# Kernel optimization log

Measured on AMD Instinct MI355X. Metric: run time of the kernel, lower is better.

## Reference

```python
import jax, jax.numpy as jnp
import numpy as np

B, S, F, D = 16384, 8, 16, 256
H, K, E, EH = 4, 16, 4, 128
ROWS = jnp.array([0, 0, 1, 1, 2, 2, 3, 3])
COLS = jnp.array([1, 3, 0, 2, 1, 3, 0, 2])
EPS = 1e-5


def setup_inputs() -> dict:
    key = jax.random.key(0)
    ks = jax.random.split(key, 16)
    s = lambda fan: 1.0 / np.sqrt(fan)
    return {
        "x": jax.random.normal(ks[0], (B, S, F), jnp.float32),
        "w_embed": jax.random.normal(ks[1], (F, D), jnp.float32) * s(F),
        "b_embed": jnp.zeros((D,), jnp.float32),
        "wq": jax.random.normal(ks[2], (D, H * K), jnp.float32) * s(D),
        "bq": jnp.zeros((H * K,), jnp.float32),
        "wk": jax.random.normal(ks[3], (D, H * K), jnp.float32) * s(D),
        "bk": jnp.zeros((H * K,), jnp.float32),
        "wv": jax.random.normal(ks[4], (D, H * K), jnp.float32) * s(D),
        "bv": jnp.zeros((H * K,), jnp.float32),
        "wo": jax.random.normal(ks[5], (H * K, D), jnp.float32) * s(H * K),
        "bo": jnp.zeros((D,), jnp.float32),
        "ln1_s": jnp.ones((D,), jnp.float32),
        "ln1_b": jnp.zeros((D,), jnp.float32),
        "wg": jax.random.normal(ks[6], (D, E), jnp.float32) * s(D),
        "bg": jnp.zeros((E,), jnp.float32),
        "w1": jax.random.normal(ks[7], (E, D, EH), jnp.float32) * s(D),
        "b1": jnp.zeros((E, EH), jnp.float32),
        "w2": jax.random.normal(ks[8], (E, EH, D), jnp.float32) * s(EH),
        "b2": jnp.zeros((E, D), jnp.float32),
        "ln2_s": jnp.ones((D,), jnp.float32),
        "ln2_b": jnp.zeros((D,), jnp.float32),
        "pad_vec": jax.random.normal(ks[9], (1, 1, 1, D), jnp.float32),
        "conv_w": jax.random.normal(ks[10], (3, 3, D, D), jnp.float32) * s(9 * D),
        "conv_b": jnp.zeros((D,), jnp.float32),
        "ln3_s": jnp.ones((D,), jnp.float32),
        "ln3_b": jnp.zeros((D,), jnp.float32),
    }


def _ln(x, scale, offset):
    m = jnp.mean(x, axis=-1, keepdims=True)
    v = jnp.mean(jnp.square(x - m), axis=-1, keepdims=True)
    return scale * (x - m) * jax.lax.rsqrt(v + EPS) + offset


def reference(x, w_embed, b_embed, wq, bq, wk, bk, wv, bv, wo, bo,
              ln1_s, ln1_b, wg, bg, w1, b1, w2, b2, ln2_s, ln2_b,
              pad_vec, conv_w, conv_b, ln3_s, ln3_b):
    # Stabilizer embedding: [B,S,F] -> [B,S,D]
    h = x @ w_embed + b_embed

    # Multi-head self-attention (haiku MultiHeadAttention semantics)
    q = (h @ wq + bq).reshape(B, S, H, K) / jnp.sqrt(jnp.asarray(K, h.dtype))
    k = (h @ wk + bk).reshape(B, S, H, K)
    v = (h @ wv + bv).reshape(B, S, H, K)
    logits = jnp.einsum('bqhk,bshk->bhqs', q, k)
    attn = jax.nn.softmax(logits, axis=-1)
    ctx = jnp.einsum('bhqs,bshk->bqhk', attn, v).reshape(B, S, H * K)
    attn_out = ctx @ wo + bo
    h = _ln(h + attn_out, ln1_s, ln1_b)

    # Dense mixture-of-experts with softmax combine
    gate = jax.nn.softmax(h @ wg + bg, axis=-1)                      # [B,S,E]
    hid = jax.nn.relu(jnp.einsum('bsd,edh->ebsh', h, w1) + b1[:, None, None, :])
    exp_out = jnp.einsum('ebsh,ehd->ebsd', hid, w2) + b2[:, None, None, :]
    moe = jnp.einsum('bse,ebsd->bsd', gate, exp_out)
    h = _ln(h + moe, ln2_s, ln2_b)

    # Scatter onto 4x4 grid, 3x3 SAME conv, gather back
    grid = jnp.tile(pad_vec, (B, 4, 4, 1))
    grid = grid.at[:, ROWS, COLS, :].set(h)
    grid_out = jax.lax.conv_general_dilated(
        grid, conv_w, window_strides=(1, 1), padding='SAME',
        dimension_numbers=('NHWC', 'HWIO', 'NHWC')) + conv_b
    conv_gathered = grid_out[:, ROWS, COLS, :]
    h = _ln(h + conv_gathered, ln3_s, ln3_b)
    return h
```

## Files before the change

kernel.cpp:

```cpp
#include <hip/hip_runtime.h>


typedef short bf16x8 __attribute__((ext_vector_type(8)));
typedef float f32x4 __attribute__((ext_vector_type(4)));

union FragU { uint4 u; bf16x8 h; };

#define MFMA(a, b, c) __builtin_amdgcn_mfma_f32_16x16x32_bf16((a), (b), (c), 0, 0, 0)

__device__ __forceinline__ unsigned short f2b(float f) {
  union { float f; unsigned int u; } x; x.f = f;
  unsigned int r = x.u + 0x7FFFu + ((x.u >> 16) & 1u);
  return (unsigned short)(r >> 16);
}

constexpr int FR_QKV  = 0;
constexpr int FR_WO   = 96;
constexpr int FR_W1   = 128;
constexpr int FR_W2   = 384;
constexpr int FR_CONV = 640;
constexpr int FR_TOT  = 1280;
constexpr size_t PADC_BYTE_OFF = (size_t)FR_TOT * 1024;

constexpr int OFF_HF = 0;
constexpr int OFF_ST = 33280;
constexpr int OFF_HB = 66560;
constexpr int OFF_MB = 83456;
constexpr int OFF_CB = 116736;
constexpr int OFF_G  = 121344;
constexpr int OFF_X  = 121856;
constexpr int SMEM_BYTES = 123904;

__device__ __forceinline__ bf16x8 ldsFrag(const unsigned short* base, int elemOff) {
  FragU x; x.u = *(const uint4*)(base + elemOff); return x.h;
}
__device__ __forceinline__ bf16x8 ldw(const uint4* wsf, int frag, int l) {
  FragU x; x.u = wsf[(size_t)frag * 64 + l]; return x.h;
}

__global__ void prep_weights(const float* __restrict__ wq, const float* __restrict__ wk,
                             const float* __restrict__ wv, const float* __restrict__ wo,
                             const float* __restrict__ w1, const float* __restrict__ w2,
                             const float* __restrict__ conv_w,
                             unsigned short* __restrict__ wsb) {
  const int flat = blockIdx.x * 256 + threadIdx.x;
  const int f = flat >> 6, l = flat & 63;
  const int nl = l & 15, rq = l >> 4;
  float v[8];
  if (f < FR_WO) {
    const int g = f, nt = g >> 3, ks = g & 7, n = nt * 16 + nl;
    #pragma unroll
    for (int e = 0; e < 8; ++e) {
      const int k = ks * 32 + rq * 8 + e;
      v[e] = (n < 64) ? wq[k * 64 + n] : (n < 128) ? wk[k * 64 + n - 64] : wv[k * 64 + n - 128];
    }
  } else if (f < FR_W1) {
    const int g = f - FR_WO, nt = g >> 1, ks = g & 1, n = nt * 16 + nl;
    #pragma unroll
    for (int e = 0; e < 8; ++e) {
      const int k = ks * 32 + rq * 8 + e;
      v[e] = wo[k * 256 + n];
    }
  } else if (f < FR_W2) {
    const int g = f - FR_W1, nt = g >> 3, ks = g & 7, n = nt * 16 + nl;
    const int ee = n >> 7, hh = n & 127;
    #pragma unroll
    for (int e = 0; e < 8; ++e) {
      const int k = ks * 32 + rq * 8 + e;
      v[e] = w1[(ee * 256 + k) * 128 + hh];
    }
  } else if (f < FR_CONV) {
    const int g = f - FR_W2, nt = g >> 4, ks = g & 15, n = nt * 16 + nl;
    #pragma unroll
    for (int e = 0; e < 8; ++e) {
      const int k = ks * 32 + rq * 8 + e;
      const int ei = k >> 7, hh = k & 127;
      v[e] = w2[(ei * 128 + hh) * 256 + n];
    }
  } else {
    const int g = f - FR_CONV, tap = g >> 7, r = g & 127, nt = r >> 3, ks = r & 7;
    const int n = nt * 16 + nl;
    #pragma unroll
    for (int e = 0; e < 8; ++e) {
      const int k = ks * 32 + rq * 8 + e;
      v[e] = conv_w[(size_t)(2 * tap) * 65536 + k * 256 + n];
    }
  }
  FragU fr;
  fr.u.x = (unsigned int)f2b(v[0]) | ((unsigned int)f2b(v[1]) << 16);
  fr.u.y = (unsigned int)f2b(v[2]) | ((unsigned int)f2b(v[3]) << 16);
  fr.u.z = (unsigned int)f2b(v[4]) | ((unsigned int)f2b(v[5]) << 16);
  fr.u.w = (unsigned int)f2b(v[6]) | ((unsigned int)f2b(v[7]) << 16);
  *(uint4*)(wsb + (size_t)f * 512 + l * 8) = fr.u;
}

__global__ void padc_kernel(const float* __restrict__ pad_vec,
                            const float* __restrict__ conv_w,
                            const float* __restrict__ conv_b,
                            float* __restrict__ padc) {
  const int s = blockIdx.x;
  const int d = threadIdx.x;
  const int NP[8]    = {3, 2, 3, 4, 4, 3, 2, 3};
  const int PT[8][4] = {{7, 3, 5, -1}, {7, 3, -1, -1}, {1, 7, 5, -1}, {1, 7, 3, 5},
                        {1, 7, 3, 5},  {1, 7, 3, -1},  {1, 5, -1, -1}, {1, 3, 5, -1}};
  float acc = conv_b[d];
  for (int t = 0; t < NP[s]; ++t) {
    const float* W = conv_w + PT[s][t] * 65536;
    for (int k = 0; k < 256; ++k) acc += pad_vec[k] * W[k * 256 + d];
  }
  padc[s * 256 + d] = acc;
}

__device__ __forceinline__ void ln_dual(const float* src, float* dstF, unsigned short* dstB,
                                        const float* __restrict__ sc, const float* __restrict__ of,
                                        int wid, int l) {
  #pragma unroll
  for (int rr = 0; rr < 4; ++rr) {
    const int r = wid * 4 + rr;
    const float* row = src + r * 260;
    float v0 = row[l], v1 = row[l + 64], v2 = row[l + 128], v3 = row[l + 192];
    float s1 = v0 + v1 + v2 + v3;
    float s2 = v0 * v0 + v1 * v1 + v2 * v2 + v3 * v3;
    #pragma unroll
    for (int m = 1; m < 64; m <<= 1) { s1 += __shfl_xor(s1, m, 64); s2 += __shfl_xor(s2, m, 64); }
    const float mean = s1 * (1.0f / 256.0f);
    const float var  = s2 * (1.0f / 256.0f) - mean * mean;
    const float rstd = rsqrtf(var + 1e-5f);
    const float o0 = sc[l] * (v0 - mean) * rstd + of[l];
    const float o1 = sc[l + 64] * (v1 - mean) * rstd + of[l + 64];
    const float o2 = sc[l + 128] * (v2 - mean) * rstd + of[l + 128];
    const float o3 = sc[l + 192] * (v3 - mean) * rstd + of[l + 192];
    dstF[r * 260 + l] = o0; dstF[r * 260 + l + 64] = o1;
    dstF[r * 260 + l + 128] = o2; dstF[r * 260 + l + 192] = o3;
    dstB[r * 264 + l] = f2b(o0); dstB[r * 264 + l + 64] = f2b(o1);
    dstB[r * 264 + l + 128] = f2b(o2); dstB[r * 264 + l + 192] = f2b(o3);
  }
}

__device__ __forceinline__ void ln_out(const float* src, const float* __restrict__ sc,
                                       const float* __restrict__ of, int wid, int l,
                                       float* __restrict__ outp) {
  #pragma unroll
  for (int rr = 0; rr < 4; ++rr) {
    const int r = wid * 4 + rr;
    const float* row = src + r * 260;
    float v0 = row[l], v1 = row[l + 64], v2 = row[l + 128], v3 = row[l + 192];
    float s1 = v0 + v1 + v2 + v3;
    float s2 = v0 * v0 + v1 * v1 + v2 * v2 + v3 * v3;
    #pragma unroll
    for (int m = 1; m < 64; m <<= 1) { s1 += __shfl_xor(s1, m, 64); s2 += __shfl_xor(s2, m, 64); }
    const float mean = s1 * (1.0f / 256.0f);
    const float var  = s2 * (1.0f / 256.0f) - mean * mean;
    const float rstd = rsqrtf(var + 1e-5f);
    float* orow = outp + (size_t)r * 256;
    orow[l]       = sc[l] * (v0 - mean) * rstd + of[l];
    orow[l + 64]  = sc[l + 64] * (v1 - mean) * rstd + of[l + 64];
    orow[l + 128] = sc[l + 128] * (v2 - mean) * rstd + of[l + 128];
    orow[l + 192] = sc[l + 192] * (v3 - mean) * rstd + of[l + 192];
  }
}

__global__ __launch_bounds__(512, 2) void fused_main(
    const float* __restrict__ x,
    const float* __restrict__ w_embed, const float* __restrict__ b_embed,
    const float* __restrict__ bq, const float* __restrict__ bk, const float* __restrict__ bv,
    const float* __restrict__ bo,
    const float* __restrict__ ln1_s, const float* __restrict__ ln1_b,
    const float* __restrict__ wg, const float* __restrict__ bg,
    const float* __restrict__ b1, const float* __restrict__ b2,
    const float* __restrict__ ln2_s, const float* __restrict__ ln2_b,
    const float* __restrict__ ln3_s, const float* __restrict__ ln3_b,
    const uint4* __restrict__ wsf, const float* __restrict__ padc,
    float* __restrict__ out) {
  __shared__ __align__(16) unsigned char smem[SMEM_BYTES];
  float* sHf = (float*)(smem + OFF_HF);
  float* sSt = (float*)(smem + OFF_ST);
  float* sQ  = sSt;
  unsigned short* sHb = (unsigned short*)(smem + OFF_HB);
  unsigned short* sMb = (unsigned short*)(smem + OFF_MB);
  unsigned short* sCb = (unsigned short*)(smem + OFF_CB);
  float* sG = (float*)(smem + OFF_G);
  float* sX = (float*)(smem + OFF_X);

  const int tid = threadIdx.x;
  const int wid = tid >> 6, l = tid & 63, rq = l >> 4, nl = l & 15;

  sX[tid] = x[(size_t)blockIdx.x * 512 + tid];
  __syncthreads();

  {
    const int c = tid & 255, r0 = (tid >> 8) * 16;
    float acc[16];
    const float bb = b_embed[c];
    #pragma unroll
    for (int r = 0; r < 16; ++r) acc[r] = bb;
    #pragma unroll
    for (int k = 0; k < 16; ++k) {
      const float w = w_embed[k * 256 + c];
      #pragma unroll
      for (int r = 0; r < 16; ++r) acc[r] += sX[(r0 + r) * 16 + k] * w;
    }
    #pragma unroll
    for (int r = 0; r < 16; ++r) {
      sHf[(r0 + r) * 260 + c] = acc[r];
      sHb[(r0 + r) * 264 + c] = f2b(acc[r]);
    }
  }
  __syncthreads();

  for (int pass = 0; pass < 2; ++pass) {
    const int nt = (pass == 0) ? wid : (wid < 4 ? 8 + wid : -1);
    if (nt < 0) break;
    f32x4 a0 = {0.f, 0.f, 0.f, 0.f}, a1 = {0.f, 0.f, 0.f, 0.f};
    #pragma unroll
    for (int ks = 0; ks < 8; ++ks) {
      const bf16x8 A0 = ldsFrag(sHb, nl * 264 + ks * 32 + rq * 8);
      const bf16x8 A1 = ldsFrag(sHb, (16 + nl) * 264 + ks * 32 + rq * 8);
      const bf16x8 Bf = ldw(wsf, FR_QKV + nt * 8 + ks, l);
      a0 = MFMA(A0, Bf, a0);
      a1 = MFMA(A1, Bf, a1);
    }
    const int n = nt * 16 + nl;
    const float bias = (n < 64) ? bq[n] : (n < 128) ? bk[n - 64] : bv[n - 128];
    const float scl = (n < 64) ? 0.25f : 1.0f;
    #pragma unroll
    for (int i = 0; i < 4; ++i) {
      sQ[(rq * 4 + i) * 200 + n] = (a0[i] + bias) * scl;
      sQ[(16 + rq * 4 + i) * 200 + n] = (a1[i] + bias) * scl;
    }
  }
  __syncthreads();

  if (tid < 128) {
    const int bl = tid >> 5, hh = (tid >> 3) & 3, qi = tid & 7, rb = bl * 8;
    const float* qrow = &sQ[(rb + qi) * 200 + hh * 16];
    float qv[16];
    #pragma unroll
    for (int kk = 0; kk < 16; kk += 4) {
      const float4 q4 = *(const float4*)&qrow[kk];
      qv[kk] = q4.x; qv[kk + 1] = q4.y; qv[kk + 2] = q4.z; qv[kk + 3] = q4.w;
    }
    float lg[8];
    #pragma unroll
    for (int j = 0; j < 8; ++j) {
      const float* krow = &sQ[(rb + j) * 200 + 64 + hh * 16];
      float d = 0.f;
      #pragma unroll
      for (int kk = 0; kk < 16; kk += 4) {
        const float4 k4 = *(const float4*)&krow[kk];
        d += qv[kk] * k4.x + qv[kk + 1] * k4.y + qv[kk + 2] * k4.z + qv[kk + 3] * k4.w;
      }
      lg[j] = d;
    }
    float mx = lg[0];
    #pragma unroll
    for (int j = 1; j < 8; ++j) mx = fmaxf(mx, lg[j]);
    float ssum = 0.f;
    #pragma unroll
    for (int j = 0; j < 8; ++j) { lg[j] = __expf(lg[j] - mx); ssum += lg[j]; }
    const float inv = 1.0f / ssum;
    #pragma unroll
    for (int kk = 0; kk < 16; kk += 4) {
      float c0 = 0.f, c1 = 0.f, c2 = 0.f, c3 = 0.f;
      #pragma unroll
      for (int j = 0; j < 8; ++j) {
        const float4 v4 = *(const float4*)&sQ[(rb + j) * 200 + 128 + hh * 16 + kk];
        c0 += lg[j] * v4.x; c1 += lg[j] * v4.y; c2 += lg[j] * v4.z; c3 += lg[j] * v4.w;
      }
      const int cb = (rb + qi) * 72 + hh * 16 + kk;
      sCb[cb] = f2b(c0 * inv); sCb[cb + 1] = f2b(c1 * inv);
      sCb[cb + 2] = f2b(c2 * inv); sCb[cb + 3] = f2b(c3 * inv);
    }
  }
  __syncthreads();

  {
    #pragma unroll
    for (int j = 0; j < 2; ++j) {
      const int nt = wid * 2 + j;
      f32x4 a0 = {0.f, 0.f, 0.f, 0.f}, a1 = {0.f, 0.f, 0.f, 0.f};
      #pragma unroll
      for (int ks = 0; ks < 2; ++ks) {
        const bf16x8 A0 = ldsFrag(sCb, nl * 72 + ks * 32 + rq * 8);
        const bf16x8 A1 = ldsFrag(sCb, (16 + nl) * 72 + ks * 32 + rq * 8);
        const bf16x8 Bf = ldw(wsf, FR_WO + nt * 2 + ks, l);
        a0 = MFMA(A0, Bf, a0);
        a1 = MFMA(A1, Bf, a1);
      }
      const int n = nt * 16 + nl;
      const float bb = bo[n];
      #pragma unroll
      for (int i = 0; i < 4; ++i) {
        const int g0 = rq * 4 + i, g1 = 16 + rq * 4 + i;
        sSt[g0 * 260 + n] = a0[i] + bb + sHf[g0 * 260 + n];
        sSt[g1 * 260 + n] = a1[i] + bb + sHf[g1 * 260 + n];
      }
    }
  }
  __syncthreads();
  ln_dual(sSt, sHf, sHb, ln1_s, ln1_b, wid, l);
  __syncthreads();

  if (tid < 128) {
    const int r = tid >> 2, e = tid & 3;
    float d = bg[e];
    for (int k4 = 0; k4 < 64; ++k4) {
      const float4 h4 = *(const float4*)&sHf[r * 260 + 4 * k4];
      d += h4.x * wg[(4 * k4 + 0) * 4 + e] + h4.y * wg[(4 * k4 + 1) * 4 + e] +
           h4.z * wg[(4 * k4 + 2) * 4 + e] + h4.w * wg[(4 * k4 + 3) * 4 + e];
    }
    float mx = fmaxf(d, __shfl_xor(d, 1, 64));
    mx = fmaxf(mx, __shfl_xor(mx, 2, 64));
    const float p = __expf(d - mx);
    float ss = p + __shfl_xor(p, 1, 64);
    ss += __shfl_xor(ss, 2, 64);
    sG[r * 4 + e] = p / ss;
  }
  __syncthreads();

  {
    f32x4 acc[4][2];
    #pragma unroll
    for (int j = 0; j < 4; ++j)
      #pragma unroll
      for (int mt = 0; mt < 2; ++mt) acc[j][mt] = {0.f, 0.f, 0.f, 0.f};
    #pragma unroll
    for (int ks = 0; ks < 8; ++ks) {
      const bf16x8 A0 = ldsFrag(sHb, nl * 264 + ks * 32 + rq * 8);
      const bf16x8 A1 = ldsFrag(sHb, (16 + nl) * 264 + ks * 32 + rq * 8);
      #pragma unroll
      for (int j = 0; j < 4; ++j) {
        const bf16x8 Bf = ldw(wsf, FR_W1 + (wid * 4 + j) * 8 + ks, l);
        acc[j][0] = MFMA(A0, Bf, acc[j][0]);
        acc[j][1] = MFMA(A1, Bf, acc[j][1]);
      }
    }
    #pragma unroll
    for (int j = 0; j < 4; ++j) {
      const int n = (wid * 4 + j) * 16 + nl, e = n >> 7;
      const float b1v = b1[e * 128 + (n & 127)];
      #pragma unroll
      for (int mt = 0; mt < 2; ++mt)
        #pragma unroll
        for (int i = 0; i < 4; ++i) {
          const int gr = mt * 16 + rq * 4 + i;
          const float g = sG[gr * 4 + e];
          sMb[gr * 520 + n] = f2b(g * fmaxf(acc[j][mt][i] + b1v, 0.f));
        }
    }
  }
  __syncthreads();

  {
    f32x4 acc[2][2];
    #pragma unroll
    for (int j = 0; j < 2; ++j)
      #pragma unroll
      for (int mt = 0; mt < 2; ++mt) acc[j][mt] = {0.f, 0.f, 0.f, 0.f};
    #pragma unroll
    for (int ks = 0; ks < 16; ++ks) {
      const bf16x8 A0 = ldsFrag(sMb, nl * 520 + ks * 32 + rq * 8);
      const bf16x8 A1 = ldsFrag(sMb, (16 + nl) * 520 + ks * 32 + rq * 8);
      #pragma unroll
      for (int j = 0; j < 2; ++j) {
        const bf16x8 Bf = ldw(wsf, FR_W2 + (wid * 2 + j) * 16 + ks, l);
        acc[j][0] = MFMA(A0, Bf, acc[j][0]);
        acc[j][1] = MFMA(A1, Bf, acc[j][1]);
      }
    }
    #pragma unroll
    for (int j = 0; j < 2; ++j) {
      const int n = (wid * 2 + j) * 16 + nl;
      const float bA = b2[n], bB = b2[256 + n], bC = b2[512 + n], bD = b2[768 + n];
      #pragma unroll
      for (int mt = 0; mt < 2; ++mt)
        #pragma unroll
        for (int i = 0; i < 4; ++i) {
          const int gr = mt * 16 + rq * 4 + i;
          const float val = acc[j][mt][i] + sG[gr * 4 + 0] * bA + sG[gr * 4 + 1] * bB +
                            sG[gr * 4 + 2] * bC + sG[gr * 4 + 3] * bD + sHf[gr * 260 + n];
          sSt[gr * 260 + n] = val;
        }
    }
  }
  __syncthreads();
  ln_dual(sSt, sHf, sHb, ln2_s, ln2_b, wid, l);
  __syncthreads();

  {
    const unsigned int ENC[5] = {0x4F320FFFu, 0x54F310FFu, 0x76543210u, 0xFF764F32u, 0xFFF754F3u};
    f32x4 acc[2][2];
    #pragma unroll
    for (int j = 0; j < 2; ++j) {
      const int n = (wid * 2 + j) * 16 + nl;
      #pragma unroll
      for (int mt = 0; mt < 2; ++mt)
        #pragma unroll
        for (int i = 0; i < 4; ++i)
          acc[j][mt][i] = padc[((rq * 4 + i) & 7) * 256 + n];
    }
    #pragma unroll
    for (int tap = 0; tap < 5; ++tap) {
      const int nib = (int)((ENC[tap] >> ((nl & 7) * 4)) & 0xF);
      const bool valid = (nib != 15);
      const int srow = (nl & 8) + (nib & 7);
      #pragma unroll
      for (int ks = 0; ks < 8; ++ks) {
        FragU fa0, fa1;
        fa0.u = *(const uint4*)(sHb + srow * 264 + ks * 32 + rq * 8);
        fa1.u = *(const uint4*)(sHb + (16 + srow) * 264 + ks * 32 + rq * 8);
        if (!valid) { fa0.u = make_uint4(0, 0, 0, 0); fa1.u = make_uint4(0, 0, 0, 0); }
        #pragma unroll
        for (int j = 0; j < 2; ++j) {
          const bf16x8 Bf = ldw(wsf, FR_CONV + tap * 128 + (wid * 2 + j) * 8 + ks, l);
          acc[j][0] = MFMA(fa0.h, Bf, acc[j][0]);
          acc[j][1] = MFMA(fa1.h, Bf, acc[j][1]);
        }
      }
    }
    #pragma unroll
    for (int j = 0; j < 2; ++j) {
      const int n = (wid * 2 + j) * 16 + nl;
      #pragma unroll
      for (int mt = 0; mt < 2; ++mt)
        #pragma unroll
        for (int i = 0; i < 4; ++i) {
          const int gr = mt * 16 + rq * 4 + i;
          sSt[gr * 260 + n] = acc[j][mt][i] + sHf[gr * 260 + n];
        }
    }
  }
  __syncthreads();
  ln_out(sSt, ln3_s, ln3_b, wid, l, out + (size_t)blockIdx.x * 32 * 256);
}

extern "C" void kernel_launch(void* const* d_in, const int* in_sizes, int n_in,
                              void* d_out, int out_size, void* d_ws, size_t ws_size,
                              hipStream_t stream) {
  const float* x       = (const float*)d_in[0];
  const float* w_embed = (const float*)d_in[1];
  const float* b_embed = (const float*)d_in[2];
  const float* wq      = (const float*)d_in[3];
  const float* bq      = (const float*)d_in[4];
  const float* wk      = (const float*)d_in[5];
  const float* bk      = (const float*)d_in[6];
  const float* wv      = (const float*)d_in[7];
  const float* bv      = (const float*)d_in[8];
  const float* wo      = (const float*)d_in[9];
  const float* bo      = (const float*)d_in[10];
  const float* ln1_s   = (const float*)d_in[11];
  const float* ln1_b   = (const float*)d_in[12];
  const float* wg      = (const float*)d_in[13];
  const float* bg      = (const float*)d_in[14];
  const float* w1      = (const float*)d_in[15];
  const float* b1      = (const float*)d_in[16];
  const float* w2      = (const float*)d_in[17];
  const float* b2      = (const float*)d_in[18];
  const float* ln2_s   = (const float*)d_in[19];
  const float* ln2_b   = (const float*)d_in[20];
  const float* pad_vec = (const float*)d_in[21];
  const float* conv_w  = (const float*)d_in[22];
  const float* conv_b  = (const float*)d_in[23];
  const float* ln3_s   = (const float*)d_in[24];
  const float* ln3_b   = (const float*)d_in[25];

  unsigned short* wsb = (unsigned short*)d_ws;
  float* padc = (float*)((char*)d_ws + PADC_BYTE_OFF);

  prep_weights<<<320, 256, 0, stream>>>(wq, wk, wv, wo, w1, w2, conv_w, wsb);
  padc_kernel<<<8, 256, 0, stream>>>(pad_vec, conv_w, conv_b, padc);
  fused_main<<<4096, 512, 0, stream>>>(
      x, w_embed, b_embed, bq, bk, bv, bo, ln1_s, ln1_b, wg, bg, b1, b2,
      ln2_s, ln2_b, ln3_s, ln3_b, (const uint4*)d_ws, padc, (float*)d_out);
}
```

Before: 606.3 us.

## Keep residual activations in registers and shrink shared memory for higher occupancy

Measured after the change: 535.5 us. -11.7%, faster.

```diff
diff --git a/kernel.cpp b/kernel.cpp
--- a/kernel.cpp
+++ b/kernel.cpp
@@ -12,6 +12,9 @@
   union { float f; unsigned int u; } x; x.f = f;
   unsigned int r = x.u + 0x7FFFu + ((x.u >> 16) & 1u);
   return (unsigned short)(r >> 16);
+}
+__device__ __forceinline__ float b2f(unsigned int us) {
+  union { unsigned int u; float f; } x; x.u = us << 16; return x.f;
 }
 
 constexpr int FR_QKV  = 0;
@@ -22,20 +25,72 @@
 constexpr int FR_TOT  = 1280;
 constexpr size_t PADC_BYTE_OFF = (size_t)FR_TOT * 1024;
 
-constexpr int OFF_HF = 0;
-constexpr int OFF_ST = 33280;
-constexpr int OFF_HB = 66560;
-constexpr int OFF_MB = 83456;
-constexpr int OFF_CB = 116736;
-constexpr int OFF_G  = 121344;
-constexpr int OFF_X  = 121856;
-constexpr int SMEM_BYTES = 123904;
+constexpr int OFF_HB = 0;
+constexpr int OFF_MQ = 16896;
+constexpr int OFF_CB = 50176;
+constexpr int OFF_X  = 54784;
+constexpr int OFF_G  = 56832;
+constexpr int OFF_LN = 57344;
+constexpr int SMEM_BYTES = 59392;
 
 __device__ __forceinline__ bf16x8 ldsFrag(const unsigned short* base, int elemOff) {
   FragU x; x.u = *(const uint4*)(base + elemOff); return x.h;
 }
 __device__ __forceinline__ bf16x8 ldw(const uint4* wsf, int frag, int l) {
   FragU x; x.u = wsf[(size_t)frag * 64 + l]; return x.h;
+}
+
+__device__ __forceinline__ void ln_part(const float nv[2][2][4], float* sLN,
+                                        int wid, int rq, int nl) {
+  float p1[2][4], p2[2][4];
+  #pragma unroll
+  for (int mt = 0; mt < 2; ++mt)
+    #pragma unroll
+    for (int i = 0; i < 4; ++i) {
+      const float a = nv[0][mt][i], b = nv[1][mt][i];
+      p1[mt][i] = a + b;
+      p2[mt][i] = a * a + b * b;
+    }
+  #pragma unroll
+  for (int m = 1; m < 16; m <<= 1) {
+    #pragma unroll
+    for (int mt = 0; mt < 2; ++mt)
+      #pragma unroll
+      for (int i = 0; i < 4; ++i) {
+        p1[mt][i] += __shfl_xor(p1[mt][i], m, 64);
+        p2[mt][i] += __shfl_xor(p2[mt][i], m, 64);
+      }
+  }
+  if (nl == 0) {
+    #pragma unroll
+    for (int mt = 0; mt < 2; ++mt)
+      #pragma unroll
+      for (int i = 0; i < 4; ++i) {
+        const int row = mt * 16 + rq * 4 + i;
+        sLN[row * 16 + wid * 2]     = p1[mt][i];
+        sLN[row * 16 + wid * 2 + 1] = p2[mt][i];
+      }
+  }
+}
+
+__device__ __forceinline__ void ln_stats(const float* sLN, int rq,
+                                         float mean[2][4], float rstd[2][4]) {
+  #pragma unroll
+  for (int mt = 0; mt < 2; ++mt)
+    #pragma unroll
+    for (int i = 0; i < 4; ++i) {
+      const int row = mt * 16 + rq * 4 + i;
+      float s1 = 0.f, s2 = 0.f;
+      #pragma unroll
+      for (int w = 0; w < 8; ++w) {
+        const float2 p = *(const float2*)&sLN[row * 16 + 2 * w];
+        s1 += p.x; s2 += p.y;
+      }
+      const float m = s1 * (1.0f / 256.0f);
+      const float v = s2 * (1.0f / 256.0f) - m * m;
+      mean[mt][i] = m;
+      rstd[mt][i] = rsqrtf(v + 1e-5f);
+    }
 }
 
 __global__ void prep_weights(const float* __restrict__ wq, const float* __restrict__ wk,
@@ -98,69 +153,25 @@
                             const float* __restrict__ conv_w,
                             const float* __restrict__ conv_b,
                             float* __restrict__ padc) {
+  __shared__ float part[4][256];
   const int s = blockIdx.x;
-  const int d = threadIdx.x;
+  const int d = threadIdx.x & 255;
+  const int q = threadIdx.x >> 8;
   const int NP[8]    = {3, 2, 3, 4, 4, 3, 2, 3};
   const int PT[8][4] = {{7, 3, 5, -1}, {7, 3, -1, -1}, {1, 7, 5, -1}, {1, 7, 3, 5},
                         {1, 7, 3, 5},  {1, 7, 3, -1},  {1, 5, -1, -1}, {1, 3, 5, -1}};
-  float acc = conv_b[d];
+  float acc = 0.f;
   for (int t = 0; t < NP[s]; ++t) {
-    const float* W = conv_w + PT[s][t] * 65536;
-    for (int k = 0; k < 256; ++k) acc += pad_vec[k] * W[k * 256 + d];
-  }
-  padc[s * 256 + d] = acc;
-}
-
-__device__ __forceinline__ void ln_dual(const float* src, float* dstF, unsigned short* dstB,
-                                        const float* __restrict__ sc, const float* __restrict__ of,
-                                        int wid, int l) {
-  #pragma unroll
-  for (int rr = 0; rr < 4; ++rr) {
-    const int r = wid * 4 + rr;
-    const float* row = src + r * 260;
-    float v0 = row[l], v1 = row[l + 64], v2 = row[l + 128], v3 = row[l + 192];
-    float s1 = v0 + v1 + v2 + v3;
-    float s2 = v0 * v0 + v1 * v1 + v2 * v2 + v3 * v3;
-    #pragma unroll
-    for (int m = 1; m < 64; m <<= 1) { s1 += __shfl_xor(s1, m, 64); s2 += __shfl_xor(s2, m, 64); }
-    const float mean = s1 * (1.0f / 256.0f);
-    const float var  = s2 * (1.0f / 256.0f) - mean * mean;
-    const float rstd = rsqrtf(var + 1e-5f);
-    const float o0 = sc[l] * (v0 - mean) * rstd + of[l];
-    const float o1 = sc[l + 64] * (v1 - mean) * rstd + of[l + 64];
-    const float o2 = sc[l + 128] * (v2 - mean) * rstd + of[l + 128];
-    const float o3 = sc[l + 192] * (v3 - mean) * rstd + of[l + 192];
-    dstF[r * 260 + l] = o0; dstF[r * 260 + l + 64] = o1;
-    dstF[r * 260 + l + 128] = o2; dstF[r * 260 + l + 192] = o3;
-    dstB[r * 264 + l] = f2b(o0); dstB[r * 264 + l + 64] = f2b(o1);
-    dstB[r * 264 + l + 128] = f2b(o2); dstB[r * 264 + l + 192] = f2b(o3);
-  }
-}
-
-__device__ __forceinline__ void ln_out(const float* src, const float* __restrict__ sc,
-                                       const float* __restrict__ of, int wid, int l,
-                                       float* __restrict__ outp) {
-  #pragma unroll
-  for (int rr = 0; rr < 4; ++rr) {
-    const int r = wid * 4 + rr;
-    const float* row = src + r * 260;
-    float v0 = row[l], v1 = row[l + 64], v2 = row[l + 128], v3 = row[l + 192];
-    float s1 = v0 + v1 + v2 + v3;
-    float s2 = v0 * v0 + v1 * v1 + v2 * v2 + v3 * v3;
-    #pragma unroll
-    for (int m = 1; m < 64; m <<= 1) { s1 += __shfl_xor(s1, m, 64); s2 += __shfl_xor(s2, m, 64); }
-    const float mean = s1 * (1.0f / 256.0f);
-    const float var  = s2 * (1.0f / 256.0f) - mean * mean;
-    const float rstd = rsqrtf(var + 1e-5f);
-    float* orow = outp + (size_t)r * 256;
-    orow[l]       = sc[l] * (v0 - mean) * rstd + of[l];
-    orow[l + 64]  = sc[l + 64] * (v1 - mean) * rstd + of[l + 64];
-    orow[l + 128] = sc[l + 128] * (v2 - mean) * rstd + of[l + 128];
-    orow[l + 192] = sc[l + 192] * (v3 - mean) * rstd + of[l + 192];
-  }
-}
-
-__global__ __launch_bounds__(512, 2) void fused_main(
+    const float* W = conv_w + PT[s][t] * 65536 + q * 64 * 256;
+    const float* pv = pad_vec + q * 64;
+    for (int k = 0; k < 64; ++k) acc += pv[k] * W[k * 256 + d];
+  }
+  part[q][d] = acc;
+  __syncthreads();
+  if (q == 0) padc[s * 256 + d] = conv_b[d] + part[0][d] + part[1][d] + part[2][d] + part[3][d];
+}
+
+__global__ __launch_bounds__(512, 4) void fused_main(
     const float* __restrict__ x,
     const float* __restrict__ w_embed, const float* __restrict__ b_embed,
     const float* __restrict__ bq, const float* __restrict__ bk, const float* __restrict__ bv,
@@ -173,38 +184,48 @@
     const uint4* __restrict__ wsf, const float* __restrict__ padc,
     float* __restrict__ out) {
   __shared__ __align__(16) unsigned char smem[SMEM_BYTES];
-  float* sHf = (float*)(smem + OFF_HF);
-  float* sSt = (float*)(smem + OFF_ST);
-  float* sQ  = sSt;
   unsigned short* sHb = (unsigned short*)(smem + OFF_HB);
-  unsigned short* sMb = (unsigned short*)(smem + OFF_MB);
+  float* sQ           = (float*)(smem + OFF_MQ);
+  unsigned short* sMb = (unsigned short*)(smem + OFF_MQ);
   unsigned short* sCb = (unsigned short*)(smem + OFF_CB);
-  float* sG = (float*)(smem + OFF_G);
-  float* sX = (float*)(smem + OFF_X);
+  float* sX  = (float*)(smem + OFF_X);
+  float* sG  = (float*)(smem + OFF_G);
+  float* sLN = (float*)(smem + OFF_LN);
 
   const int tid = threadIdx.x;
   const int wid = tid >> 6, l = tid & 63, rq = l >> 4, nl = l & 15;
+  const int n0 = wid * 32 + nl, n1 = n0 + 16;
+
+  float hR[2][2][4];
+  float nv[2][2][4];
 
   sX[tid] = x[(size_t)blockIdx.x * 512 + tid];
   __syncthreads();
 
   {
-    const int c = tid & 255, r0 = (tid >> 8) * 16;
-    float acc[16];
-    const float bb = b_embed[c];
-    #pragma unroll
-    for (int r = 0; r < 16; ++r) acc[r] = bb;
+    float wc0[16], wc1[16];
     #pragma unroll
     for (int k = 0; k < 16; ++k) {
-      const float w = w_embed[k * 256 + c];
-      #pragma unroll
-      for (int r = 0; r < 16; ++r) acc[r] += sX[(r0 + r) * 16 + k] * w;
-    }
-    #pragma unroll
-    for (int r = 0; r < 16; ++r) {
-      sHf[(r0 + r) * 260 + c] = acc[r];
-      sHb[(r0 + r) * 264 + c] = f2b(acc[r]);
-    }
+      wc0[k] = w_embed[k * 256 + n0];
+      wc1[k] = w_embed[k * 256 + n1];
+    }
+    const float bb0 = b_embed[n0], bb1 = b_embed[n1];
+    #pragma unroll
+    for (int mt = 0; mt < 2; ++mt)
+      #pragma unroll
+      for (int i = 0; i < 4; ++i) {
+        const int gr = mt * 16 + rq * 4 + i;
+        float a0 = bb0, a1 = bb1;
+        #pragma unroll
+        for (int kk = 0; kk < 4; ++kk) {
+          const float4 xv = *(const float4*)&sX[gr * 16 + kk * 4];
+          a0 += xv.x * wc0[4 * kk] + xv.y * wc0[4 * kk + 1] + xv.z * wc0[4 * kk + 2] + xv.w * wc0[4 * kk + 3];
+          a1 += xv.x * wc1[4 * kk] + xv.y * wc1[4 * kk + 1] + xv.z * wc1[4 * kk + 2] + xv.w * wc1[4 * kk + 3];
+        }
+        hR[0][mt][i] = a0; hR[1][mt][i] = a1;
+        sHb[gr * 264 + n0] = f2b(a0);
+        sHb[gr * 264 + n1] = f2b(a1);
+      }
   }
   __syncthreads();
 
@@ -287,27 +308,45 @@
         a0 = MFMA(A0, Bf, a0);
         a1 = MFMA(A1, Bf, a1);
       }
-      const int n = nt * 16 + nl;
-      const float bb = bo[n];
-      #pragma unroll
-      for (int i = 0; i < 4; ++i) {
-        const int g0 = rq * 4 + i, g1 = 16 + rq * 4 + i;
-        sSt[g0 * 260 + n] = a0[i] + bb + sHf[g0 * 260 + n];
-        sSt[g1 * 260 + n] = a1[i] + bb + sHf[g1 * 260 + n];
-      }
-    }
-  }
-  __syncthreads();
-  ln_dual(sSt, sHf, sHb, ln1_s, ln1_b, wid, l);
+      const float bb = bo[j ? n1 : n0];
+      #pragma unroll
+      for (int i = 0; i < 4; ++i) {
+        nv[j][0][i] = a0[i] + bb + hR[j][0][i];
+        nv[j][1][i] = a1[i] + bb + hR[j][1][i];
+      }
+    }
+  }
+  ln_part(nv, sLN, wid, rq, nl);
+  __syncthreads();
+  {
+    float mean[2][4], rstd[2][4];
+    ln_stats(sLN, rq, mean, rstd);
+    const float sc0 = ln1_s[n0], sc1 = ln1_s[n1], of0 = ln1_b[n0], of1 = ln1_b[n1];
+    #pragma unroll
+    for (int mt = 0; mt < 2; ++mt)
+      #pragma unroll
+      for (int i = 0; i < 4; ++i) {
+        const int gr = mt * 16 + rq * 4 + i;
+        const float o0 = sc0 * (nv[0][mt][i] - mean[mt][i]) * rstd[mt][i] + of0;
+        const float o1 = sc1 * (nv[1][mt][i] - mean[mt][i]) * rstd[mt][i] + of1;
+        hR[0][mt][i] = o0; hR[1][mt][i] = o1;
+        sHb[gr * 264 + n0] = f2b(o0);
+        sHb[gr * 264 + n1] = f2b(o1);
+      }
+  }
   __syncthreads();
 
   if (tid < 128) {
     const int r = tid >> 2, e = tid & 3;
     float d = bg[e];
-    for (int k4 = 0; k4 < 64; ++k4) {
-      const float4 h4 = *(const float4*)&sHf[r * 260 + 4 * k4];
-      d += h4.x * wg[(4 * k4 + 0) * 4 + e] + h4.y * wg[(4 * k4 + 1) * 4 + e] +
-           h4.z * wg[(4 * k4 + 2) * 4 + e] + h4.w * wg[(4 * k4 + 3) * 4 + e];
+    #pragma unroll 4
+    for (int k8 = 0; k8 < 32; ++k8) {
+      const uint4 u = *(const uint4*)(sHb + r * 264 + k8 * 8);
+      const float* wp = &wg[k8 * 32 + e];
+      d += b2f(u.x & 0xffffu) * wp[0]  + b2f(u.x >> 16) * wp[4]
+         + b2f(u.y & 0xffffu) * wp[8]  + b2f(u.y >> 16) * wp[12]
+         + b2f(u.z & 0xffffu) * wp[16] + b2f(u.z >> 16) * wp[20]
+         + b2f(u.w & 0xffffu) * wp[24] + b2f(u.w >> 16) * wp[28];
     }
     float mx = fmaxf(d, __shfl_xor(d, 1, 64));
     mx = fmaxf(mx, __shfl_xor(mx, 2, 64));
@@ -370,21 +409,36 @@
     }
     #pragma unroll
     for (int j = 0; j < 2; ++j) {
-      const int n = (wid * 2 + j) * 16 + nl;
+      const int n = j ? n1 : n0;
       const float bA = b2[n], bB = b2[256 + n], bC = b2[512 + n], bD = b2[768 + n];
       #pragma unroll
       for (int mt = 0; mt < 2; ++mt)
         #pragma unroll
         for (int i = 0; i < 4; ++i) {
           const int gr = mt * 16 + rq * 4 + i;
-          const float val = acc[j][mt][i] + sG[gr * 4 + 0] * bA + sG[gr * 4 + 1] * bB +
-                            sG[gr * 4 + 2] * bC + sG[gr * 4 + 3] * bD + sHf[gr * 260 + n];
-          sSt[gr * 260 + n] = val;
+          nv[j][mt][i] = acc[j][mt][i] + sG[gr * 4 + 0] * bA + sG[gr * 4 + 1] * bB +
+                         sG[gr * 4 + 2] * bC + sG[gr * 4 + 3] * bD + hR[j][mt][i];
         }
     }
   }
-  __syncthreads();
-  ln_dual(sSt, sHf, sHb, ln2_s, ln2_b, wid, l);
+  ln_part(nv, sLN, wid, rq, nl);
+  __syncthreads();
+  {
+    float mean[2][4], rstd[2][4];
+    ln_stats(sLN, rq, mean, rstd);
+    const float sc0 = ln2_s[n0], sc1 = ln2_s[n1], of0 = ln2_b[n0], of1 = ln2_b[n1];
+    #pragma unroll
+    for (int mt = 0; mt < 2; ++mt)
+      #pragma unroll
+      for (int i = 0; i < 4; ++i) {
+        const int gr = mt * 16 + rq * 4 + i;
+        const float o0 = sc0 * (nv[0][mt][i] - mean[mt][i]) * rstd[mt][i] + of0;
+        const float o1 = sc1 * (nv[1][mt][i] - mean[mt][i]) * rstd[mt][i] + of1;
+        hR[0][mt][i] = o0; hR[1][mt][i] = o1;
+        sHb[gr * 264 + n0] = f2b(o0);
+        sHb[gr * 264 + n1] = f2b(o1);
+      }
+  }
   __syncthreads();
 
   {
@@ -392,7 +446,7 @@
     f32x4 acc[2][2];
     #pragma unroll
     for (int j = 0; j < 2; ++j) {
-      const int n = (wid * 2 + j) * 16 + nl;
+      const int n = j ? n1 : n0;
       #pragma unroll
       for (int mt = 0; mt < 2; ++mt)
         #pragma unroll
@@ -419,19 +473,30 @@
       }
     }
     #pragma unroll
-    for (int j = 0; j < 2; ++j) {
-      const int n = (wid * 2 + j) * 16 + nl;
+    for (int j = 0; j < 2; ++j)
       #pragma unroll
       for (int mt = 0; mt < 2; ++mt)
         #pragma unroll
-        for (int i = 0; i < 4; ++i) {
-          const int gr = mt * 16 + rq * 4 + i;
-          sSt[gr * 260 + n] = acc[j][mt][i] + sHf[gr * 260 + n];
-        }
-    }
-  }
-  __syncthreads();
-  ln_out(sSt, ln3_s, ln3_b, wid, l, out + (size_t)blockIdx.x * 32 * 256);
+        for (int i = 0; i < 4; ++i)
+          nv[j][mt][i] = acc[j][mt][i] + hR[j][mt][i];
+  }
+  ln_part(nv, sLN, wid, rq, nl);
+  __syncthreads();
+
+  {
+    float mean[2][4], rstd[2][4];
+    ln_stats(sLN, rq, mean, rstd);
+    const float sc0 = ln3_s[n0], sc1 = ln3_s[n1], of0 = ln3_b[n0], of1 = ln3_b[n1];
+    float* ob = out + (size_t)blockIdx.x * 32 * 256;
+    #pragma unroll
+    for (int mt = 0; mt < 2; ++mt)
+      #pragma unroll
+      for (int i = 0; i < 4; ++i) {
+        const int gr = mt * 16 + rq * 4 + i;
+        ob[gr * 256 + n0] = sc0 * (nv[0][mt][i] - mean[mt][i]) * rstd[mt][i] + of0;
+        ob[gr * 256 + n1] = sc1 * (nv[1][mt][i] - mean[mt][i]) * rstd[mt][i] + of1;
+      }
+  }
 }
 
 extern "C" void kernel_launch(void* const* d_in, const int* in_sizes, int n_in,
@@ -468,7 +533,7 @@
   float* padc = (float*)((char*)d_ws + PADC_BYTE_OFF);
 
   prep_weights<<<320, 256, 0, stream>>>(wq, wk, wv, wo, w1, w2, conv_w, wsb);
-  padc_kernel<<<8, 256, 0, stream>>>(pad_vec, conv_w, conv_b, padc);
+  padc_kernel<<<8, 1024, 0, stream>>>(pad_vec, conv_w, conv_b, padc);
   fused_main<<<4096, 512, 0, stream>>>(
       x, w_embed, b_embed, bq, bk, bv, bo, ln1_s, ln1_b, wg, bg, b1, b2,
       ln2_s, ln2_b, ln3_s, ln3_b, (const uint4*)d_ws, padc, (float*)d_out);
```
